# Kernel tuning notes

Hardware: AMD Instinct MI355X
Metric: run time of the kernel (lower is better)

Reference implementation:

```python
import jax, jax.numpy as jnp
import numpy as np

B, S, D = 8, 2048, 1024  # batch, seq_len, emb_dim == qkv_dim
NEG = -999999.0  # module uses -999999 instead of -inf


def setup_inputs() -> dict:
    key = jax.random.key(0)
    ks = jax.random.split(key, 4)
    inputs = jax.random.normal(ks[0], (B, S, D), dtype=jnp.float32)
    # causal mask, flax attention layout [B, 1, S, S]
    causal = jnp.tril(jnp.ones((S, S), dtype=bool))
    mask = jnp.broadcast_to(causal, (B, 1, S, S))
    scale = 1.0 / np.sqrt(D)
    Wq = jax.random.normal(ks[1], (D, D), dtype=jnp.float32) * scale
    Wk = jax.random.normal(ks[2], (D, D), dtype=jnp.float32) * scale
    Wv = jax.random.normal(ks[3], (D, D), dtype=jnp.float32) * scale
    z = jnp.zeros((D,), dtype=jnp.float32)
    return {"inputs": inputs, "mask": mask, "Wq": Wq, "bq": z, "Wk": Wk,
            "bk": z, "Wv": Wv, "bv": z}


def reference(inputs, mask, Wq, bq, Wk, bk, Wv, bv):
    q = inputs @ Wq + bq  # [B,S,D]
    k = inputs @ Wk + bk
    v = inputs @ Wv + bv
    depth = q.shape[-1]
    q = q / jnp.sqrt(jnp.asarray(depth, q.dtype))
    attn = jnp.einsum('bqd,bkd->bqk', q, k)  # [B,S,S]
    attn = jnp.where(jnp.squeeze(mask, axis=1), attn, NEG)
    attn = jax.nn.softmax(attn, axis=-1)
    return attn @ v  # [B,S,D]
```

## Files before the change

### kernel.cpp

```cpp
#include <hip/hip_runtime.h>
#include <hip/hip_bf16.h>
#include <cstdint>

#define S_LEN 2048
#define D_DIM 1024
#define NB 8

typedef __attribute__((ext_vector_type(8))) short bf16x8;
typedef __attribute__((ext_vector_type(4))) float f32x4;

__device__ __forceinline__ unsigned short f2bf(float f) {
  union { float f; unsigned u; } x; x.f = f;
  unsigned r = x.u + 0x7fffu + ((x.u >> 16) & 1u);
  return (unsigned short)(r >> 16);
}
__device__ __forceinline__ void gload16(const void* g, void* l) {
  __builtin_amdgcn_global_load_lds((const __attribute__((address_space(1))) void*)g,
                                   (__attribute__((address_space(3))) void*)l, 16, 0, 0);
}

__global__ __launch_bounds__(256)
void cvt_f32_bf16(const float* __restrict__ in, unsigned short* __restrict__ out, int n4) {
  int i = blockIdx.x * blockDim.x + threadIdx.x;
  if (i >= n4) return;
  float4 v = reinterpret_cast<const float4*>(in)[i];
  ushort4 o;
  o.x = f2bf(v.x); o.y = f2bf(v.y); o.z = f2bf(v.z); o.w = f2bf(v.w);
  reinterpret_cast<ushort4*>(out)[i] = o;
}

__global__ __launch_bounds__(256)
void transpose_f32_bf16(const float* __restrict__ in, unsigned short* __restrict__ out,
                        int rows, int cols) {
  __shared__ unsigned short tile[32][33];
  int bx = blockIdx.x * 32, by = blockIdx.y * 32;
  int tx = threadIdx.x, ty = threadIdx.y;
  #pragma unroll
  for (int i = ty; i < 32; i += 8)
    tile[i][tx] = f2bf(in[(size_t)(by + i) * cols + bx + tx]);
  __syncthreads();
  #pragma unroll
  for (int i = ty; i < 32; i += 8)
    out[(size_t)(bx + i) * rows + by + tx] = tile[tx][i];
}

__global__ __launch_bounds__(256)
void transpose_bf16(const unsigned short* __restrict__ in, unsigned short* __restrict__ out,
                    int ldin, int ldout, long zin, long zout) {
  __shared__ unsigned short tile[32][33];
  const unsigned short* ip = in + (size_t)blockIdx.z * zin;
  unsigned short* op = out + (size_t)blockIdx.z * zout;
  int bx = blockIdx.x * 32, by = blockIdx.y * 32;
  int tx = threadIdx.x, ty = threadIdx.y;
  #pragma unroll
  for (int i = ty; i < 32; i += 8)
    tile[i][tx] = ip[(size_t)(by + i) * ldin + bx + tx];
  __syncthreads();
  #pragma unroll
  for (int i = ty; i < 32; i += 8)
    op[(size_t)(bx + i) * ldout + by + tx] = tile[tx][i];
}

template<int MODE>
__global__ __launch_bounds__(512, 2)
void gemm8(const unsigned short* __restrict__ Aall, const unsigned short* __restrict__ Btall,
           void* __restrict__ Call, int Kd, int lda, int ldb, int ldc,
           long sAz, long sBz, long sCz,
           const float* __restrict__ b0, const float* __restrict__ b1,
           const float* __restrict__ b2, float* __restrict__ rowsum, int ntn) {
  __shared__ __align__(16) unsigned short As[4][8192];
  __shared__ __align__(16) unsigned short Bs[4][8192];
  int nwg = gridDim.x, bid = blockIdx.x;
  int wg = (bid & 7) * (nwg >> 3) + (bid >> 3);
  int tm = wg / ntn, tn = wg % ntn;
  int z = blockIdx.z;
  if (MODE == 1 && tn > tm) return;
  const unsigned short* A  = Aall  + (size_t)z * sAz;
  const unsigned short* Bt = Btall + (size_t)z * sBz;
  int m0 = tm * 256, n0 = tn * 256;
  int t = threadIdx.x, lane = t & 63, w = t >> 6;
  int wr = w >> 2, wc = w & 3;
  int lr = lane & 15, lq = lane >> 4;
  int nkt = (MODE == 2) ? (tm + 1) * 8 : (Kd >> 5);

  int offA[8], offB[4];
  #pragma unroll
  for (int mi = 0; mi < 8; ++mi) {
    int row = wr * 128 + mi * 16 + lr;
    offA[mi] = row * 32 + ((lq ^ ((row >> 1) & 3)) * 8);
  }
  #pragma unroll
  for (int ni = 0; ni < 4; ++ni) {
    int row = wc * 64 + ni * 16 + lr;
    offB[ni] = row * 32 + ((lq ^ ((row >> 1) & 3)) * 8);
  }
  int srow[2], soff[2];
  #pragma unroll
  for (int c = 0; c < 2; ++c) {
    int r = c * 128 + w * 16 + (lane >> 2);
    srow[c] = r;
    soff[c] = ((lane & 3) ^ ((r >> 1) & 3)) * 8;
  }

  f32x4 acc[8][4];
  f32x4 zero4 = {0.f, 0.f, 0.f, 0.f};
  #pragma unroll
  for (int mi = 0; mi < 8; ++mi)
    #pragma unroll
    for (int ni = 0; ni < 4; ++ni) acc[mi][ni] = zero4;

  auto stgA = [&](int buf, int kt2) {
    int kb = kt2 * 32;
    #pragma unroll
    for (int c = 0; c < 2; ++c)
      gload16(A + (size_t)(m0 + srow[c]) * lda + kb + soff[c], &As[buf][c * 4096 + w * 512]);
  };
  auto stgB = [&](int buf, int kt2) {
    int kb = kt2 * 32;
    #pragma unroll
    for (int c = 0; c < 2; ++c)
      gload16(Bt + (size_t)(n0 + srow[c]) * ldb + kb + soff[c], &Bs[buf][c * 4096 + w * 512]);
  };

  stgA(0, 0); stgB(0, 0); stgA(1, 1); stgB(1, 1);
  asm volatile("s_waitcnt vmcnt(4)" ::: "memory");
  __builtin_amdgcn_s_barrier();

  for (int kt = 0; kt < nkt; ++kt) {
    const int bcur = kt & 3, bpre = (kt + 2) & 3;
    const bool stg = (kt + 2 < nkt);
    const unsigned short* Ac = &As[bcur][0];
    const unsigned short* Bc = &Bs[bcur][0];
    bf16x8 af[4], bfv[4];

    #pragma unroll
    for (int i = 0; i < 4; ++i) af[i]  = *reinterpret_cast<const bf16x8*>(&Ac[offA[i]]);
    #pragma unroll
    for (int i = 0; i < 4; ++i) bfv[i] = *reinterpret_cast<const bf16x8*>(&Bc[offB[i]]);
    if (stg) stgA(bpre, kt + 2);
    __builtin_amdgcn_s_barrier();
    asm volatile("s_waitcnt lgkmcnt(0)" ::: "memory");
    __builtin_amdgcn_sched_barrier(0);
    __builtin_amdgcn_s_setprio(1);
    #pragma unroll
    for (int i = 0; i < 4; ++i)
      #pragma unroll
      for (int j = 0; j < 4; ++j)
        acc[i][j] = __builtin_amdgcn_mfma_f32_16x16x32_bf16(af[i], bfv[j], acc[i][j], 0, 0, 0);
    __builtin_amdgcn_s_setprio(0);
    __builtin_amdgcn_s_barrier();

    #pragma unroll
    for (int i = 0; i < 4; ++i) af[i] = *reinterpret_cast<const bf16x8*>(&Ac[offA[4 + i]]);
    if (stg) stgB(bpre, kt + 2);
    if (kt + 2 < nkt)      asm volatile("s_waitcnt vmcnt(4)" ::: "memory");
    else if (kt + 1 < nkt) asm volatile("s_waitcnt vmcnt(0)" ::: "memory");
    __builtin_amdgcn_s_barrier();
    asm volatile("s_waitcnt lgkmcnt(0)" ::: "memory");
    __builtin_amdgcn_sched_barrier(0);
    __builtin_amdgcn_s_setprio(1);
    #pragma unroll
    for (int i = 0; i < 4; ++i)
      #pragma unroll
      for (int j = 0; j < 4; ++j)
        acc[4 + i][j] = __builtin_amdgcn_mfma_f32_16x16x32_bf16(af[i], bfv[j], acc[4 + i][j], 0, 0, 0);
    __builtin_amdgcn_s_setprio(0);
    __builtin_amdgcn_s_barrier();
  }
  __syncthreads();

  unsigned short* ep = &As[0][0] + w * 4096;
  int lq4 = lq << 4;

  if (MODE == 0) {
    unsigned short* C = (unsigned short*)Call;
    #pragma unroll
    for (int mh = 0; mh < 2; ++mh) {
      #pragma unroll
      for (int mi2 = 0; mi2 < 4; ++mi2)
        #pragma unroll
        for (int ni = 0; ni < 4; ++ni) {
          int col = ni * 16 + lr;
          int gcol = n0 + wc * 64 + col;
          float bb, sc;
          if (gcol < 1024)      { bb = b0[gcol];        sc = 0.03125f; }
          else if (gcol < 2048) { bb = b1[gcol - 1024]; sc = 1.0f; }
          else                  { bb = b2[gcol - 2048]; sc = 1.0f; }
          #pragma unroll
          for (int j = 0; j < 4; ++j) {
            int lrow = mi2 * 16 + lq * 4 + j;
            ep[lrow * 64 + (col ^ lq4)] = f2bf((acc[mh * 4 + mi2][ni][j] + bb) * sc);
          }
        }
      #pragma unroll
      for (int pass = 0; pass < 8; ++pass) {
        int rrow = pass * 8 + (lane >> 3);
        int c8 = (lane & 7) * 8;
        int sw = ((rrow >> 2) & 3) << 4;
        bf16x8 vv = *reinterpret_cast<const bf16x8*>(&ep[rrow * 64 + (c8 ^ sw)]);
        int grow = m0 + wr * 128 + mh * 64 + rrow;
        *reinterpret_cast<bf16x8*>(&C[(size_t)grow * ldc + n0 + wc * 64 + c8]) = vv;
      }
      asm volatile("s_waitcnt lgkmcnt(0)" ::: "memory");
    }
  } else if (MODE == 1) {
    unsigned short* C = (unsigned short*)Call + (size_t)z * sCz;
    float* rs = rowsum + z * S_LEN;
    #pragma unroll
    for (int mh = 0; mh < 2; ++mh) {
      #pragma unroll
      for (int mi2 = 0; mi2 < 4; ++mi2)
        #pragma unroll
        for (int j = 0; j < 4; ++j) {
          int lrow = mi2 * 16 + lq * 4 + j;
          int grow = m0 + wr * 128 + mh * 64 + lrow;
          float partial = 0.f;
          #pragma unroll
          for (int ni = 0; ni < 4; ++ni) {
            int col = ni * 16 + lr;
            int gcol = n0 + wc * 64 + col;
            float e = (gcol <= grow) ? __expf(acc[mh * 4 + mi2][ni][j]) : 0.f;
            partial += e;
            ep[lrow * 64 + (col ^ lq4)] = f2bf(e);
          }
          #pragma unroll
          for (int off = 1; off < 16; off <<= 1) partial += __shfl_xor(partial, off);
          if (lr == 0) atomicAdd(&rs[grow], partial);
        }
      #pragma unroll
      for (int pass = 0; pass < 8; ++pass) {
        int rrow = pass * 8 + (lane >> 3);
        int c8 = (lane & 7) * 8;
        int sw = ((rrow >> 2) & 3) << 4;
        bf16x8 vv = *reinterpret_cast<const bf16x8*>(&ep[rrow * 64 + (c8 ^ sw)]);
        int grow = m0 + wr * 128 + mh * 64 + rrow;
        *reinterpret_cast<bf16x8*>(&C[(size_t)grow * ldc + n0 + wc * 64 + c8]) = vv;
      }
      asm volatile("s_waitcnt lgkmcnt(0)" ::: "memory");
    }
  } else {
    float* C = (float*)Call + (size_t)z * sCz;
    const float* rs = rowsum + z * S_LEN;
    #pragma unroll
    for (int mi = 0; mi < 8; ++mi)
      #pragma unroll
      for (int j = 0; j < 4; ++j) {
        int row = m0 + wr * 128 + mi * 16 + lq * 4 + j;
        float inv = 1.f / rs[row];
        #pragma unroll
        for (int ni = 0; ni < 4; ++ni) {
          int col = n0 + wc * 64 + ni * 16 + lr;
          C[(size_t)row * ldc + col] = acc[mi][ni][j] * inv;
        }
      }
  }
}

extern "C" void kernel_launch(void* const* d_in, const int* in_sizes, int n_in,
                              void* d_out, int out_size, void* d_ws, size_t ws_size,
                              hipStream_t stream) {
  (void)in_sizes; (void)n_in; (void)out_size; (void)ws_size;
  const float* X  = (const float*)d_in[0];
  const float* Wq = (const float*)d_in[2];
  const float* bq = (const float*)d_in[3];
  const float* Wk = (const float*)d_in[4];
  const float* bk = (const float*)d_in[5];
  const float* Wv = (const float*)d_in[6];
  const float* bv = (const float*)d_in[7];

  char* ws = (char*)d_ws;
  unsigned short* Xb  = (unsigned short*)(ws);
  unsigned short* Wt  = (unsigned short*)(ws + 33554432L);
  float*          Rs  = (float*)(ws + 33554432L);
  unsigned short* QKV = (unsigned short*)(ws + 39845888L);
  unsigned short* Pb  = (unsigned short*)(ws + 140509184L);
  unsigned short* Vt  = Xb;

  cvt_f32_bf16<<<16384, 256, 0, stream>>>(X, Xb, (NB * S_LEN * D_DIM) / 4);
  dim3 tb(32, 8);
  transpose_f32_bf16<<<dim3(32, 32), tb, 0, stream>>>(Wq, Wt + 0L * 1048576L, D_DIM, D_DIM);
  transpose_f32_bf16<<<dim3(32, 32), tb, 0, stream>>>(Wk, Wt + 1L * 1048576L, D_DIM, D_DIM);
  transpose_f32_bf16<<<dim3(32, 32), tb, 0, stream>>>(Wv, Wt + 2L * 1048576L, D_DIM, D_DIM);
  gemm8<0><<<dim3(64 * 12, 1, 1), 512, 0, stream>>>(Xb, Wt, (void*)QKV,
      D_DIM, D_DIM, D_DIM, 3 * D_DIM,
      0L, 0L, 0L, bq, bk, bv, nullptr, 12);
  hipMemsetAsync(Rs, 0, NB * S_LEN * sizeof(float), stream);
  gemm8<1><<<dim3(64, 1, NB), 512, 0, stream>>>(QKV, QKV + 1024, (void*)Pb,
      D_DIM, 3 * D_DIM, 3 * D_DIM, S_LEN,
      (long)S_LEN * 3 * D_DIM, (long)S_LEN * 3 * D_DIM, (long)S_LEN * S_LEN,
      nullptr, nullptr, nullptr, Rs, 8);
  transpose_bf16<<<dim3(32, 64, NB), tb, 0, stream>>>(QKV + 2048, Vt,
      3 * D_DIM, S_LEN, (long)S_LEN * 3 * D_DIM, (long)D_DIM * S_LEN);
  gemm8<2><<<dim3(32, 1, NB), 512, 0, stream>>>(Pb, Vt, d_out,
      S_LEN, S_LEN, S_LEN, D_DIM,
      (long)S_LEN * S_LEN, (long)D_DIM * S_LEN, (long)S_LEN * D_DIM,
      nullptr, nullptr, nullptr, Rs, 4);
}
```

Baseline: 328.0 us.

## Switch GEMM to 32x32x16 MFMA tiles and deepen prefetch to three stages

Replaces the 16x16x32 bf16 MFMA micro-tiles with 32x32x16 MFMAs. This changes the LDS fragment offsets, the accumulator layout and all three epilogues (bias/scale store, exp+rowsum, normalize) to match the new row/column mapping. Fewer, larger MFMAs need fewer LDS fragment reads per FLOP. Prefetch distance also grows from 2 to 3 of the 4 LDS buffers, with adjusted vmcnt waits, to hide more global latency. The risks are the new swizzle pattern causing bank conflicts and the tighter buffer reuse causing race hazards.

Measured after the change: 352.1 us. 7.4% more time.

```diff
diff --git a/kernel.cpp b/kernel.cpp
--- a/kernel.cpp
+++ b/kernel.cpp
@@ -7,7 +7,7 @@
 #define NB 8
 
 typedef __attribute__((ext_vector_type(8))) short bf16x8;
-typedef __attribute__((ext_vector_type(4))) float f32x4;
+typedef __attribute__((ext_vector_type(16))) float f32x16;
 
 __device__ __forceinline__ unsigned short f2bf(float f) {
   union { float f; unsigned u; } x; x.f = f;
@@ -80,20 +80,26 @@
   int m0 = tm * 256, n0 = tn * 256;
   int t = threadIdx.x, lane = t & 63, w = t >> 6;
   int wr = w >> 2, wc = w & 3;
-  int lr = lane & 15, lq = lane >> 4;
+  int lc = lane & 31, hi = lane >> 5;
   int nkt = (MODE == 2) ? (tm + 1) * 8 : (Kd >> 5);
 
   int offA[8], offB[4];
   #pragma unroll
-  for (int mi = 0; mi < 8; ++mi) {
-    int row = wr * 128 + mi * 16 + lr;
-    offA[mi] = row * 32 + ((lq ^ ((row >> 1) & 3)) * 8);
-  }
-  #pragma unroll
-  for (int ni = 0; ni < 4; ++ni) {
-    int row = wc * 64 + ni * 16 + lr;
-    offB[ni] = row * 32 + ((lq ^ ((row >> 1) & 3)) * 8);
-  }
+  for (int mi = 0; mi < 4; ++mi)
+    #pragma unroll
+    for (int ks = 0; ks < 2; ++ks) {
+      int row = wr * 128 + mi * 32 + lc;
+      int slot = ks * 2 + hi;
+      offA[mi * 2 + ks] = row * 32 + ((slot ^ ((row >> 1) & 3)) * 8);
+    }
+  #pragma unroll
+  for (int ni = 0; ni < 2; ++ni)
+    #pragma unroll
+    for (int ks = 0; ks < 2; ++ks) {
+      int row = wc * 64 + ni * 32 + lc;
+      int slot = ks * 2 + hi;
+      offB[ni * 2 + ks] = row * 32 + ((slot ^ ((row >> 1) & 3)) * 8);
+    }
   int srow[2], soff[2];
   #pragma unroll
   for (int c = 0; c < 2; ++c) {
@@ -102,12 +108,13 @@
     soff[c] = ((lane & 3) ^ ((r >> 1) & 3)) * 8;
   }
 
-  f32x4 acc[8][4];
-  f32x4 zero4 = {0.f, 0.f, 0.f, 0.f};
-  #pragma unroll
-  for (int mi = 0; mi < 8; ++mi)
-    #pragma unroll
-    for (int ni = 0; ni < 4; ++ni) acc[mi][ni] = zero4;
+  f32x16 acc[4][2];
+  #pragma unroll
+  for (int mi = 0; mi < 4; ++mi)
+    #pragma unroll
+    for (int ni = 0; ni < 2; ++ni)
+      #pragma unroll
+      for (int r = 0; r < 16; ++r) acc[mi][ni][r] = 0.f;
 
   auto stgA = [&](int buf, int kt2) {
     int kb = kt2 * 32;
@@ -122,22 +129,22 @@
       gload16(Bt + (size_t)(n0 + srow[c]) * ldb + kb + soff[c], &Bs[buf][c * 4096 + w * 512]);
   };
 
-  stgA(0, 0); stgB(0, 0); stgA(1, 1); stgB(1, 1);
-  asm volatile("s_waitcnt vmcnt(4)" ::: "memory");
+  stgA(0, 0); stgB(0, 0); stgA(1, 1); stgB(1, 1); stgA(2, 2); stgB(2, 2);
+  asm volatile("s_waitcnt vmcnt(8)" ::: "memory");
   __builtin_amdgcn_s_barrier();
 
   for (int kt = 0; kt < nkt; ++kt) {
-    const int bcur = kt & 3, bpre = (kt + 2) & 3;
-    const bool stg = (kt + 2 < nkt);
-    const unsigned short* Ac = &As[bcur][0];
-    const unsigned short* Bc = &Bs[bcur][0];
-    bf16x8 af[4], bfv[4];
-
-    #pragma unroll
-    for (int i = 0; i < 4; ++i) af[i]  = *reinterpret_cast<const bf16x8*>(&Ac[offA[i]]);
-    #pragma unroll
-    for (int i = 0; i < 4; ++i) bfv[i] = *reinterpret_cast<const bf16x8*>(&Bc[offB[i]]);
-    if (stg) stgA(bpre, kt + 2);
+    const int bcur = kt & 3, bpre = (kt + 3) & 3;
+    const bool stg = (kt + 3 < nkt);
+    const unsigned short* Ac = As[bcur];
+    const unsigned short* Bc = Bs[bcur];
+    bf16x8 afr[4], bfr[2];
+
+    #pragma unroll
+    for (int i = 0; i < 4; ++i) afr[i] = *reinterpret_cast<const bf16x8*>(&Ac[offA[i * 2]]);
+    #pragma unroll
+    for (int i = 0; i < 2; ++i) bfr[i] = *reinterpret_cast<const bf16x8*>(&Bc[offB[i * 2]]);
+    if (stg) stgA(bpre, kt + 3);
     __builtin_amdgcn_s_barrier();
     asm volatile("s_waitcnt lgkmcnt(0)" ::: "memory");
     __builtin_amdgcn_sched_barrier(0);
@@ -145,16 +152,19 @@
     #pragma unroll
     for (int i = 0; i < 4; ++i)
       #pragma unroll
-      for (int j = 0; j < 4; ++j)
-        acc[i][j] = __builtin_amdgcn_mfma_f32_16x16x32_bf16(af[i], bfv[j], acc[i][j], 0, 0, 0);
+      for (int j = 0; j < 2; ++j)
+        acc[i][j] = __builtin_amdgcn_mfma_f32_32x32x16_bf16(afr[i], bfr[j], acc[i][j], 0, 0, 0);
     __builtin_amdgcn_s_setprio(0);
     __builtin_amdgcn_s_barrier();
 
     #pragma unroll
-    for (int i = 0; i < 4; ++i) af[i] = *reinterpret_cast<const bf16x8*>(&Ac[offA[4 + i]]);
-    if (stg) stgB(bpre, kt + 2);
-    if (kt + 2 < nkt)      asm volatile("s_waitcnt vmcnt(4)" ::: "memory");
-    else if (kt + 1 < nkt) asm volatile("s_waitcnt vmcnt(0)" ::: "memory");
+    for (int i = 0; i < 4; ++i) afr[i] = *reinterpret_cast<const bf16x8*>(&Ac[offA[i * 2 + 1]]);
+    #pragma unroll
+    for (int i = 0; i < 2; ++i) bfr[i] = *reinterpret_cast<const bf16x8*>(&Bc[offB[i * 2 + 1]]);
+    if (stg) stgB(bpre, kt + 3);
+    if (kt + 4 <= nkt)      asm volatile("s_waitcnt vmcnt(8)" ::: "memory");
+    else if (kt + 3 <= nkt) asm volatile("s_waitcnt vmcnt(4)" ::: "memory");
+    else if (kt + 2 <= nkt) asm volatile("s_waitcnt vmcnt(0)" ::: "memory");
     __builtin_amdgcn_s_barrier();
     asm volatile("s_waitcnt lgkmcnt(0)" ::: "memory");
     __builtin_amdgcn_sched_barrier(0);
@@ -162,95 +172,97 @@
     #pragma unroll
     for (int i = 0; i < 4; ++i)
       #pragma unroll
-      for (int j = 0; j < 4; ++j)
-        acc[4 + i][j] = __builtin_amdgcn_mfma_f32_16x16x32_bf16(af[i], bfv[j], acc[4 + i][j], 0, 0, 0);
+      for (int j = 0; j < 2; ++j)
+        acc[i][j] = __builtin_amdgcn_mfma_f32_32x32x16_bf16(afr[i], bfr[j], acc[i][j], 0, 0, 0);
     __builtin_amdgcn_s_setprio(0);
     __builtin_amdgcn_s_barrier();
   }
   __syncthreads();
 
-  unsigned short* ep = &As[0][0] + w * 4096;
-  int lq4 = lq << 4;
+  unsigned short* ep = &As[0][0] + w * 2048;
 
   if (MODE == 0) {
     unsigned short* C = (unsigned short*)Call;
     #pragma unroll
-    for (int mh = 0; mh < 2; ++mh) {
-      #pragma unroll
-      for (int mi2 = 0; mi2 < 4; ++mi2)
+    for (int mi = 0; mi < 4; ++mi) {
+      #pragma unroll
+      for (int ni = 0; ni < 2; ++ni) {
+        int col = ni * 32 + lc;
+        int gcol = n0 + wc * 64 + col;
+        float bb, sc;
+        if (gcol < 1024)      { bb = b0[gcol];        sc = 0.03125f; }
+        else if (gcol < 2048) { bb = b1[gcol - 1024]; sc = 1.0f; }
+        else                  { bb = b2[gcol - 2048]; sc = 1.0f; }
         #pragma unroll
-        for (int ni = 0; ni < 4; ++ni) {
-          int col = ni * 16 + lr;
-          int gcol = n0 + wc * 64 + col;
-          float bb, sc;
-          if (gcol < 1024)      { bb = b0[gcol];        sc = 0.03125f; }
-          else if (gcol < 2048) { bb = b1[gcol - 1024]; sc = 1.0f; }
-          else                  { bb = b2[gcol - 2048]; sc = 1.0f; }
-          #pragma unroll
-          for (int j = 0; j < 4; ++j) {
-            int lrow = mi2 * 16 + lq * 4 + j;
-            ep[lrow * 64 + (col ^ lq4)] = f2bf((acc[mh * 4 + mi2][ni][j] + bb) * sc);
-          }
+        for (int r = 0; r < 16; ++r) {
+          int lrow = (r & 3) + 8 * (r >> 2) + 4 * hi;
+          int cp = (((col >> 3) ^ (lrow & 7)) << 3) + (col & 7);
+          ep[lrow * 64 + cp] = f2bf((acc[mi][ni][r] + bb) * sc);
         }
-      #pragma unroll
-      for (int pass = 0; pass < 8; ++pass) {
-        int rrow = pass * 8 + (lane >> 3);
-        int c8 = (lane & 7) * 8;
-        int sw = ((rrow >> 2) & 3) << 4;
-        bf16x8 vv = *reinterpret_cast<const bf16x8*>(&ep[rrow * 64 + (c8 ^ sw)]);
-        int grow = m0 + wr * 128 + mh * 64 + rrow;
-        *reinterpret_cast<bf16x8*>(&C[(size_t)grow * ldc + n0 + wc * 64 + c8]) = vv;
       }
       asm volatile("s_waitcnt lgkmcnt(0)" ::: "memory");
+      __builtin_amdgcn_sched_barrier(0);
+      #pragma unroll
+      for (int p = 0; p < 4; ++p) {
+        int rrow = p * 8 + (lane >> 3);
+        bf16x8 vv = *reinterpret_cast<const bf16x8*>(
+            &ep[rrow * 64 + (((lane & 7) ^ (rrow & 7)) << 3)]);
+        int grow = m0 + wr * 128 + mi * 32 + rrow;
+        *reinterpret_cast<bf16x8*>(&C[(size_t)grow * ldc + n0 + wc * 64 + (lane & 7) * 8]) = vv;
+      }
+      asm volatile("s_waitcnt lgkmcnt(0)" ::: "memory");
+      __builtin_amdgcn_sched_barrier(0);
     }
   } else if (MODE == 1) {
     unsigned short* C = (unsigned short*)Call + (size_t)z * sCz;
     float* rs = rowsum + z * S_LEN;
     #pragma unroll
-    for (int mh = 0; mh < 2; ++mh) {
-      #pragma unroll
-      for (int mi2 = 0; mi2 < 4; ++mi2)
+    for (int mi = 0; mi < 4; ++mi) {
+      #pragma unroll
+      for (int r = 0; r < 16; ++r) {
+        int lrow = (r & 3) + 8 * (r >> 2) + 4 * hi;
+        int grow = m0 + wr * 128 + mi * 32 + lrow;
+        float partial = 0.f;
         #pragma unroll
-        for (int j = 0; j < 4; ++j) {
-          int lrow = mi2 * 16 + lq * 4 + j;
-          int grow = m0 + wr * 128 + mh * 64 + lrow;
-          float partial = 0.f;
-          #pragma unroll
-          for (int ni = 0; ni < 4; ++ni) {
-            int col = ni * 16 + lr;
-            int gcol = n0 + wc * 64 + col;
-            float e = (gcol <= grow) ? __expf(acc[mh * 4 + mi2][ni][j]) : 0.f;
-            partial += e;
-            ep[lrow * 64 + (col ^ lq4)] = f2bf(e);
-          }
-          #pragma unroll
-          for (int off = 1; off < 16; off <<= 1) partial += __shfl_xor(partial, off);
-          if (lr == 0) atomicAdd(&rs[grow], partial);
+        for (int ni = 0; ni < 2; ++ni) {
+          int col = ni * 32 + lc;
+          int gcol = n0 + wc * 64 + col;
+          float e = (gcol <= grow) ? __expf(acc[mi][ni][r]) : 0.f;
+          partial += e;
+          int cp = (((col >> 3) ^ (lrow & 7)) << 3) + (col & 7);
+          ep[lrow * 64 + cp] = f2bf(e);
         }
-      #pragma unroll
-      for (int pass = 0; pass < 8; ++pass) {
-        int rrow = pass * 8 + (lane >> 3);
-        int c8 = (lane & 7) * 8;
-        int sw = ((rrow >> 2) & 3) << 4;
-        bf16x8 vv = *reinterpret_cast<const bf16x8*>(&ep[rrow * 64 + (c8 ^ sw)]);
-        int grow = m0 + wr * 128 + mh * 64 + rrow;
-        *reinterpret_cast<bf16x8*>(&C[(size_t)grow * ldc + n0 + wc * 64 + c8]) = vv;
+        #pragma unroll
+        for (int off = 1; off < 32; off <<= 1) partial += __shfl_xor(partial, off);
+        if (lc == 0) atomicAdd(&rs[grow], partial);
       }
       asm volatile("s_waitcnt lgkmcnt(0)" ::: "memory");
+      __builtin_amdgcn_sched_barrier(0);
+      #pragma unroll
+      for (int p = 0; p < 4; ++p) {
+        int rrow = p * 8 + (lane >> 3);
+        bf16x8 vv = *reinterpret_cast<const bf16x8*>(
+            &ep[rrow * 64 + (((lane & 7) ^ (rrow & 7)) << 3)]);
+        int grow = m0 + wr * 128 + mi * 32 + rrow;
+        *reinterpret_cast<bf16x8*>(&C[(size_t)grow * ldc + n0 + wc * 64 + (lane & 7) * 8]) = vv;
+      }
+      asm volatile("s_waitcnt lgkmcnt(0)" ::: "memory");
+      __builtin_amdgcn_sched_barrier(0);
     }
   } else {
     float* C = (float*)Call + (size_t)z * sCz;
     const float* rs = rowsum + z * S_LEN;
     #pragma unroll
-    for (int mi = 0; mi < 8; ++mi)
-      #pragma unroll
-      for (int j = 0; j < 4; ++j) {
-        int row = m0 + wr * 128 + mi * 16 + lq * 4 + j;
-        float inv = 1.f / rs[row];
+    for (int mi = 0; mi < 4; ++mi)
+      #pragma unroll
+      for (int r = 0; r < 16; ++r) {
+        int lrow = (r & 3) + 8 * (r >> 2) + 4 * hi;
+        int grow = m0 + wr * 128 + mi * 32 + lrow;
+        float inv = 1.f / rs[grow];
         #pragma unroll
-        for (int ni = 0; ni < 4; ++ni) {
-          int col = n0 + wc * 64 + ni * 16 + lr;
-          C[(size_t)row * ldc + col] = acc[mi][ni][j] * inv;
+        for (int ni = 0; ni < 2; ++ni) {
+          int gcol = n0 + wc * 64 + ni * 32 + lc;
+          C[(size_t)grow * ldc + gcol] = acc[mi][ni][r] * inv;
         }
       }
   }
```
